# Performance work log

Hardware: AMD Instinct MI355X
Metric: run time of the kernel (lower is better)

The kernel has to match this reference:

```python
import jax, jax.numpy as jnp
import numpy as np

N = 50000
E = 800000
IN_DIM = 128
OUT_DIM = 128
EDGE_DIM = 3
H = 4
HD = OUT_DIM // H  # 32
SCALE = HD ** -0.5


def setup_inputs() -> dict:
    key = jax.random.key(0)
    ks = jax.random.split(key, 10)
    x = jax.random.normal(ks[0], (N, IN_DIM), dtype=jnp.float32)
    edge_index = jax.random.randint(ks[1], (2, E), 0, N, dtype=jnp.int64)
    edge_attr = jax.random.normal(ks[2], (E, EDGE_DIM), dtype=jnp.float32)
    s = 1.0 / np.sqrt(IN_DIM)
    Wq = jax.random.normal(ks[3], (IN_DIM, H * HD), dtype=jnp.float32) * s
    Wk = jax.random.normal(ks[4], (IN_DIM, H * HD), dtype=jnp.float32) * s
    Wv = jax.random.normal(ks[5], (IN_DIM, H * HD), dtype=jnp.float32) * s
    We = jax.random.normal(ks[6], (EDGE_DIM, H), dtype=jnp.float32) * (1.0 / np.sqrt(EDGE_DIM))
    Wo = jax.random.normal(ks[7], (H * HD, OUT_DIM), dtype=jnp.float32) * (1.0 / np.sqrt(H * HD))
    bo = jnp.zeros((OUT_DIM,), dtype=jnp.float32)
    Wm = jax.random.normal(ks[8], (IN_DIM + OUT_DIM, OUT_DIM), dtype=jnp.float32) * (1.0 / np.sqrt(IN_DIM + OUT_DIM))
    bm = jnp.zeros((OUT_DIM,), dtype=jnp.float32)
    return {"x": x, "edge_index": edge_index, "edge_attr": edge_attr,
            "Wq": Wq, "Wk": Wk, "Wv": Wv, "We": We, "Wo": Wo, "bo": bo,
            "Wm": Wm, "bm": bm}


def reference(x, edge_index, edge_attr, Wq, Wk, Wv, We, Wo, bo, Wm, bm):
    n = x.shape[0]
    src = edge_index[0]
    dst = edge_index[1]
    Q = (x @ Wq).reshape(n, H, HD)
    K = (x @ Wk).reshape(n, H, HD)
    V = (x @ Wv).reshape(n, H, HD)
    edge_bias = edge_attr @ We                                  # [E, H]
    attn = jnp.sum(Q[dst] * K[src], axis=-1) * SCALE + edge_bias  # [E, H]
    attn = jnp.where(attn >= 0, attn, 0.2 * attn)               # leaky_relu(0.2)
    # NOTE: original uses a single GLOBAL max over all edges/heads for stability
    attn_exp = jnp.exp(attn - jnp.max(attn))
    attn_sum = jax.ops.segment_sum(attn_exp, dst, num_segments=n)  # [N, H]
    attn_norm = attn_exp / jnp.maximum(attn_sum[dst], 1e-12)
    # dropout disabled (eval mode)
    weighted_V = V[src] * attn_norm[:, :, None]                 # [E, H, HD]
    agg = jax.ops.segment_sum(weighted_V, dst, num_segments=n)  # [N, H, HD]
    agg = agg.reshape(n, H * HD) @ Wo + bo                      # [N, OUT]
    h = jnp.concatenate([x, agg], axis=1) @ Wm + bm
    return jax.nn.relu(h)
```

## Files before the change

kernel.cpp:

```cpp
#include <hip/hip_runtime.h>
#include <hip/hip_bf16.h>
#include <math.h>

#define NN 50000
#define NE 800000
#define DIM 128
#define NH 4
#define HD 32
#define EH (NE * NH)
#define ATTN_SCALE 0.17677669529663687f
#define MTILE 64
#define GEMM_BLOCKS 782
#define NBKT 98
#define PTS 2048
#define PBLKS 391
#define HBLKS 104

typedef unsigned int uint;
typedef unsigned short ushort;
typedef __attribute__((ext_vector_type(8))) short short8;
typedef __attribute__((ext_vector_type(4))) float f32x4;

__device__ inline ushort f2bf(float f) {
    __hip_bfloat16 h = __float2bfloat16(f);
    return *(ushort*)&h;
}
__device__ inline float bflo(uint u) { return __uint_as_float(u << 16); }
__device__ inline float bfhi(uint u) { return __uint_as_float(u & 0xffff0000u); }

__global__ __launch_bounds__(256) void prep_x_kernel(
    const float* __restrict__ x, ushort* __restrict__ xb)
{
    const int i = blockIdx.x * 256 + threadIdx.x;
    const float4 v = ((const float4*)x)[i];
    ushort4 o;
    o.x = f2bf(v.x); o.y = f2bf(v.y); o.z = f2bf(v.z); o.w = f2bf(v.w);
    ((ushort4*)xb)[i] = o;
}

__global__ __launch_bounds__(128) void prep_wx_kernel(
    const float* __restrict__ Wo, const float* __restrict__ Wm,
    float* __restrict__ Wx)
{
    const int r = blockIdx.x, j = threadIdx.x;
    float acc = 0.f;
    for (int t = 0; t < 128; ++t)
        acc = fmaf(Wo[r * 128 + t], Wm[(128 + t) * 128 + j], acc);
    Wx[r * 128 + j] = acc;
}

__global__ __launch_bounds__(128) void prep_bias_kernel(
    const float* __restrict__ bo, const float* __restrict__ bm,
    const float* __restrict__ Wm, float* __restrict__ bprime)
{
    const int j = threadIdx.x;
    float acc = bm[j];
    for (int t = 0; t < 128; ++t)
        acc = fmaf(bo[t], Wm[(128 + t) * 128 + j], acc);
    bprime[j] = acc;
}

__global__ __launch_bounds__(256) void pack_qkv_kernel(
    const float* __restrict__ Wq, const float* __restrict__ Wk,
    const float* __restrict__ Wv, short* __restrict__ Bp)
{
    const int idx = blockIdx.x * 256 + threadIdx.x;
    const int j = idx & 7, lane = (idx >> 3) & 63;
    const int rest = idx >> 9;
    const int nt = rest % 24, kc = rest / 24;
    const int k = kc * 32 + (lane >> 4) * 8 + j;
    const int n = nt * 16 + (lane & 15);
    const float* W = (n < 128) ? Wq : (n < 256 ? Wk : Wv);
    Bp[idx] = (short)f2bf(W[k * 128 + (n & 127)]);
}

__global__ __launch_bounds__(256) void pack_out_kernel(
    const float* __restrict__ Wm, const float* __restrict__ Wx,
    short* __restrict__ Bp)
{
    const int idx = blockIdx.x * 256 + threadIdx.x;
    const int j = idx & 7, lane = (idx >> 3) & 63;
    const int rest = idx >> 9;
    const int nt = rest & 7, kc = rest >> 3;
    const int k = kc * 32 + (lane >> 4) * 8 + j;
    const int n = nt * 16 + (lane & 15);
    const float v = (k < 128) ? Wm[k * 128 + n] : Wx[(k - 128) * 128 + n];
    Bp[idx] = (short)f2bf(v);
}

__global__ __launch_bounds__(128) void bkt_zero_kernel(int* __restrict__ bkt_cnt)
{
    if (threadIdx.x < 128) bkt_cnt[threadIdx.x] = 0;
}

__global__ __launch_bounds__(256) void bkt_hist_kernel(
    const int* __restrict__ dst, int* __restrict__ bkt_cnt)
{
    __shared__ int c[NBKT];
    const int tid = threadIdx.x;
    if (tid < NBKT) c[tid] = 0;
    __syncthreads();
    for (int e = blockIdx.x * 256 + tid; e < NE; e += HBLKS * 256)
        atomicAdd(&c[dst[e] >> 9], 1);
    __syncthreads();
    if (tid < NBKT && c[tid]) atomicAdd(&bkt_cnt[tid], c[tid]);
}

__global__ void bkt_scan_kernel(const int* __restrict__ bkt_cnt,
                                int* __restrict__ bkt_base,
                                int* __restrict__ bkt_cursor,
                                int* __restrict__ rowptr)
{
    if (threadIdx.x == 0) {
        int run = 0;
        for (int b = 0; b < NBKT; ++b) {
            bkt_base[b] = run;
            bkt_cursor[b] = run;
            run += bkt_cnt[b];
        }
        bkt_base[NBKT] = run;
        rowptr[NN] = run;
    }
}

__global__ __launch_bounds__(256) void partition_kernel(
    const int* __restrict__ src, const int* __restrict__ dst,
    const float* __restrict__ edge_attr, const float* __restrict__ We,
    int* __restrict__ bkt_cursor,
    int* __restrict__ psrc, int* __restrict__ pdst, float* __restrict__ peb)
{
    __shared__ int cnt[NBKT], rbase[NBKT], cnt2[NBKT];
    const int tid = threadIdx.x;
    if (tid < NBKT) cnt[tid] = 0;
    __syncthreads();
    const int e0 = blockIdx.x * PTS;
    #pragma unroll
    for (int it = 0; it < 8; ++it) {
        const int e = e0 + it * 256 + tid;
        if (e < NE) atomicAdd(&cnt[dst[e] >> 9], 1);
    }
    __syncthreads();
    if (tid < NBKT) {
        rbase[tid] = cnt[tid] ? atomicAdd(&bkt_cursor[tid], cnt[tid]) : 0;
        cnt2[tid] = 0;
    }
    __syncthreads();
    #pragma unroll
    for (int it = 0; it < 8; ++it) {
        const int e = e0 + it * 256 + tid;
        if (e < NE) {
            const int d = dst[e];
            const int b = d >> 9;
            const int r = atomicAdd(&cnt2[b], 1);
            const int pos = rbase[b] + r;
            psrc[pos] = src[e];
            pdst[pos] = d;
            const float a0 = edge_attr[e * 3 + 0];
            const float a1 = edge_attr[e * 3 + 1];
            const float a2 = edge_attr[e * 3 + 2];
            float4 eb;
            eb.x = a0 * We[0] + a1 * We[4] + a2 * We[8];
            eb.y = a0 * We[1] + a1 * We[5] + a2 * We[9];
            eb.z = a0 * We[2] + a1 * We[6] + a2 * We[10];
            eb.w = a0 * We[3] + a1 * We[7] + a2 * We[11];
            *(float4*)(peb + (size_t)pos * 4) = eb;
        }
    }
}

__global__ __launch_bounds__(256) void bucket_csr_kernel(
    const int* __restrict__ bkt_base,
    const int* __restrict__ psrc, const int* __restrict__ pdst,
    const float* __restrict__ peb,
    int* __restrict__ rowptr,
    int* __restrict__ srcp, float* __restrict__ eb_csr)
{
    __shared__ int cnt[512];
    __shared__ int pre[512];
    __shared__ int sc[256];
    const int tid = threadIdx.x;
    const int b = blockIdx.x;
    const int base = bkt_base[b];
    const int n = bkt_base[b + 1] - base;
    const int node0 = b << 9;

    cnt[tid] = 0; cnt[tid + 256] = 0;
    __syncthreads();
    for (int i = base + tid; i < base + n; i += 256)
        atomicAdd(&cnt[pdst[i] - node0], 1);
    __syncthreads();

    const int pair = cnt[2 * tid] + cnt[2 * tid + 1];
    sc[tid] = pair;
    __syncthreads();
    for (int off = 1; off < 256; off <<= 1) {
        const int v = (tid >= off) ? sc[tid - off] : 0;
        __syncthreads();
        sc[tid] += v;
        __syncthreads();
    }
    const int ex = sc[tid] - pair;
    pre[2 * tid] = base + ex;
    pre[2 * tid + 1] = base + ex + cnt[2 * tid];
    __syncthreads();

    for (int l = tid; l < 512; l += 256) {
        const int g = node0 + l;
        if (g < NN) rowptr[g] = pre[l];
    }
    __syncthreads();

    for (int i = base + tid; i < base + n; i += 256) {
        const int d = pdst[i];
        const int pos = atomicAdd(&pre[d - node0], 1);
        srcp[pos] = psrc[i];
        *(float4*)(eb_csr + (size_t)pos * 4) =
            *(const float4*)(peb + (size_t)i * 4);
    }
}

__global__ __launch_bounds__(256) void qkv_mfma_kernel(
    const ushort* __restrict__ xb, const short* __restrict__ Bp,
    ushort* __restrict__ Qb, ushort* __restrict__ Kb, ushort* __restrict__ Vb)
{
    const int wave = threadIdx.x >> 6;
    const int lane = threadIdx.x & 63;
    const int m = lane & 15, quad = lane >> 4;
    const int row0w = blockIdx.x * MTILE + wave * 16;
    const int arow = row0w + m;
    const bool rowok = arow < NN;

    short8 a[4];
    #pragma unroll
    for (int kc = 0; kc < 4; ++kc)
        a[kc] = rowok ? *(const short8*)(xb + (size_t)arow * 128 + kc * 32 + quad * 8)
                      : (short8)(0);

    const int NT = 24;
    for (int nt = 0; nt < NT; nt += 2) {
        f32x4 acc0 = {0.f, 0.f, 0.f, 0.f}, acc1 = {0.f, 0.f, 0.f, 0.f};
        #pragma unroll
        for (int kc = 0; kc < 4; ++kc) {
            const short8 b0 = *(const short8*)(Bp + ((size_t)(kc * NT + nt) * 64 + lane) * 8);
            const short8 b1 = *(const short8*)(Bp + ((size_t)(kc * NT + nt + 1) * 64 + lane) * 8);
            acc0 = __builtin_amdgcn_mfma_f32_16x16x32_bf16(a[kc], b0, acc0, 0, 0, 0);
            acc1 = __builtin_amdgcn_mfma_f32_16x16x32_bf16(a[kc], b1, acc1, 0, 0, 0);
        }
        #pragma unroll
        for (int t = 0; t < 2; ++t) {
            const f32x4 acc = t ? acc1 : acc0;
            const int c = (nt + t) * 16 + m;
            ushort* dstp_ = (c < 128) ? Qb : (c < 256 ? Kb : Vb);
            const int lc = c & 127;
            #pragma unroll
            for (int g = 0; g < 4; ++g) {
                const int r = row0w + quad * 4 + g;
                if (r < NN) dstp_[(size_t)r * 128 + lc] = f2bf(acc[g]);
            }
        }
    }
}

__global__ __launch_bounds__(256) void out_mfma_kernel(
    const ushort* __restrict__ xb, const ushort* __restrict__ aggb,
    const short* __restrict__ Bp, const float* __restrict__ bprime,
    float* __restrict__ out)
{
    const int wave = threadIdx.x >> 6;
    const int lane = threadIdx.x & 63;
    const int m = lane & 15, quad = lane >> 4;
    const int row0w = blockIdx.x * MTILE + wave * 16;
    const int arow = row0w + m;
    const bool rowok = arow < NN;

    short8 a[8];
    #pragma unroll
    for (int kc = 0; kc < 4; ++kc)
        a[kc] = rowok ? *(const short8*)(xb + (size_t)arow * 128 + kc * 32 + quad * 8)
                      : (short8)(0);
    #pragma unroll
    for (int kc = 0; kc < 4; ++kc)
        a[4 + kc] = rowok ? *(const short8*)(aggb + (size_t)arow * 128 + kc * 32 + quad * 8)
                          : (short8)(0);

    const int NT = 8;
    for (int nt = 0; nt < NT; nt += 2) {
        f32x4 acc0 = {0.f, 0.f, 0.f, 0.f}, acc1 = {0.f, 0.f, 0.f, 0.f};
        #pragma unroll
        for (int kc = 0; kc < 8; ++kc) {
            const short8 b0 = *(const short8*)(Bp + ((size_t)(kc * NT + nt) * 64 + lane) * 8);
            const short8 b1 = *(const short8*)(Bp + ((size_t)(kc * NT + nt + 1) * 64 + lane) * 8);
            acc0 = __builtin_amdgcn_mfma_f32_16x16x32_bf16(a[kc], b0, acc0, 0, 0, 0);
            acc1 = __builtin_amdgcn_mfma_f32_16x16x32_bf16(a[kc], b1, acc1, 0, 0, 0);
        }
        #pragma unroll
        for (int t = 0; t < 2; ++t) {
            const f32x4 acc = t ? acc1 : acc0;
            const int c = (nt + t) * 16 + m;
            const float bb = bprime[c];
            #pragma unroll
            for (int g = 0; g < 4; ++g) {
                const int r = row0w + quad * 4 + g;
                if (r < NN) out[(size_t)r * 128 + c] = fmaxf(acc[g] + bb, 0.f);
            }
        }
    }
}

__global__ __launch_bounds__(256) void attn_agg_kernel(
    const ushort* __restrict__ Qb, const ushort* __restrict__ Kb,
    const ushort* __restrict__ Vb,
    const int* __restrict__ rowptr, const int* __restrict__ srcp,
    const float* __restrict__ eb_csr, ushort* __restrict__ aggb)
{
    const int tid = threadIdx.x;
    const int d = blockIdx.x * 4 + (tid >> 6);
    const int jj = tid & 63;
    const int h = jj >> 4;
    const int begin = rowptr[d];
    const int end   = rowptr[d + 1];

    const uint uq = *(const uint*)(Qb + (size_t)d * DIM + 2 * jj);
    const float q0 = bflo(uq), q1 = bfhi(uq);

    float ss0 = 0.f, ss1 = 0.f, ss2 = 0.f, ss3 = 0.f;
    float x0 = 0.f, x1 = 0.f, x2 = 0.f, x3 = 0.f;
    float y0 = 0.f, y1 = 0.f, y2 = 0.f, y3 = 0.f;

    int p = begin;
    for (; p + 4 <= end; p += 4) {
        const int s0 = srcp[p + 0];
        const int s1 = srcp[p + 1];
        const int s2 = srcp[p + 2];
        const int s3 = srcp[p + 3];
        const uint k0 = *(const uint*)(Kb + (size_t)s0 * DIM + 2 * jj);
        const uint k1 = *(const uint*)(Kb + (size_t)s1 * DIM + 2 * jj);
        const uint k2 = *(const uint*)(Kb + (size_t)s2 * DIM + 2 * jj);
        const uint k3 = *(const uint*)(Kb + (size_t)s3 * DIM + 2 * jj);
        float p0 = fmaf(q0, bflo(k0), q1 * bfhi(k0));
        float p1 = fmaf(q0, bflo(k1), q1 * bfhi(k1));
        float p2 = fmaf(q0, bflo(k2), q1 * bfhi(k2));
        float p3 = fmaf(q0, bflo(k3), q1 * bfhi(k3));
        #pragma unroll
        for (int m2 = 1; m2 <= 8; m2 <<= 1) {
            p0 += __shfl_xor(p0, m2);
            p1 += __shfl_xor(p1, m2);
            p2 += __shfl_xor(p2, m2);
            p3 += __shfl_xor(p3, m2);
        }
        float a0 = fmaf(p0, ATTN_SCALE, eb_csr[(size_t)(p + 0) * 4 + h]);
        float a1 = fmaf(p1, ATTN_SCALE, eb_csr[(size_t)(p + 1) * 4 + h]);
        float a2 = fmaf(p2, ATTN_SCALE, eb_csr[(size_t)(p + 2) * 4 + h]);
        float a3 = fmaf(p3, ATTN_SCALE, eb_csr[(size_t)(p + 3) * 4 + h]);
        a0 = (a0 >= 0.f) ? a0 : 0.2f * a0;
        a1 = (a1 >= 0.f) ? a1 : 0.2f * a1;
        a2 = (a2 >= 0.f) ? a2 : 0.2f * a2;
        a3 = (a3 >= 0.f) ? a3 : 0.2f * a3;
        const float w0 = __expf(a0);
        const float w1 = __expf(a1);
        const float w2 = __expf(a2);
        const float w3 = __expf(a3);
        const uint v0 = *(const uint*)(Vb + (size_t)s0 * DIM + 2 * jj);
        const uint v1 = *(const uint*)(Vb + (size_t)s1 * DIM + 2 * jj);
        const uint v2 = *(const uint*)(Vb + (size_t)s2 * DIM + 2 * jj);
        const uint v3 = *(const uint*)(Vb + (size_t)s3 * DIM + 2 * jj);
        ss0 += w0; ss1 += w1; ss2 += w2; ss3 += w3;
        x0 = fmaf(w0, bflo(v0), x0); y0 = fmaf(w0, bfhi(v0), y0);
        x1 = fmaf(w1, bflo(v1), x1); y1 = fmaf(w1, bfhi(v1), y1);
        x2 = fmaf(w2, bflo(v2), x2); y2 = fmaf(w2, bfhi(v2), y2);
        x3 = fmaf(w3, bflo(v3), x3); y3 = fmaf(w3, bfhi(v3), y3);
    }
    for (; p < end; ++p) {
        const int s = srcp[p];
        const uint uk = *(const uint*)(Kb + (size_t)s * DIM + 2 * jj);
        float part = fmaf(q0, bflo(uk), q1 * bfhi(uk));
        part += __shfl_xor(part, 1);
        part += __shfl_xor(part, 2);
        part += __shfl_xor(part, 4);
        part += __shfl_xor(part, 8);
        float a = fmaf(part, ATTN_SCALE, eb_csr[(size_t)p * 4 + h]);
        a = (a >= 0.f) ? a : 0.2f * a;
        const float w = __expf(a);
        const uint uv = *(const uint*)(Vb + (size_t)s * DIM + 2 * jj);
        ss0 += w;
        x0 = fmaf(w, bflo(uv), x0);
        y0 = fmaf(w, bfhi(uv), y0);
    }
    const float ssum = (ss0 + ss1) + (ss2 + ss3);
    const float inv = 1.f / fmaxf(ssum, 1e-12f);
    const float ax = ((x0 + x1) + (x2 + x3)) * inv;
    const float ay = ((y0 + y1) + (y2 + y3)) * inv;
    const uint packed = (uint)f2bf(ax) | ((uint)f2bf(ay) << 16);
    *(uint*)(aggb + (size_t)d * DIM + 2 * jj) = packed;
}

extern "C" void kernel_launch(void* const* d_in, const int* in_sizes, int n_in,
                              void* d_out, int out_size, void* d_ws, size_t ws_size,
                              hipStream_t stream)
{
    const float* x         = (const float*)d_in[0];
    const int*   edge_idx  = (const int*)d_in[1];
    const float* edge_attr = (const float*)d_in[2];
    const float* Wq        = (const float*)d_in[3];
    const float* Wk        = (const float*)d_in[4];
    const float* Wv        = (const float*)d_in[5];
    const float* We        = (const float*)d_in[6];
    const float* Wo        = (const float*)d_in[7];
    const float* bo        = (const float*)d_in[8];
    const float* Wm        = (const float*)d_in[9];
    const float* bm        = (const float*)d_in[10];
    float* out = (float*)d_out;

    const int* src = edge_idx;
    const int* dst = edge_idx + NE;

    ushort* xb   = (ushort*)d_ws;
    ushort* Qb   = xb + (size_t)NN * DIM;
    ushort* Kb   = Qb + (size_t)NN * DIM;
    ushort* Vb   = Kb + (size_t)NN * DIM;
    ushort* aggb = Vb + (size_t)NN * DIM;
    int*   psrc     = (int*)(aggb + (size_t)NN * DIM);
    int*   pdst     = psrc + NE;
    float* peb      = (float*)(pdst + NE);
    float* eb_csr   = peb + (size_t)EH;
    float* Wx       = eb_csr + (size_t)EH;
    float* bprime   = Wx + 16384;
    short* BpQKV    = (short*)(bprime + 128);
    short* BpOut    = BpQKV + 49152;
    int*   rowptr   = (int*)(BpOut + 32768);
    int*   srcp     = rowptr + 50048;
    int*   bkt_cnt    = srcp + NE;
    int*   bkt_base   = bkt_cnt + 128;
    int*   bkt_cursor = bkt_base + 128;

    prep_x_kernel<<<(NN * DIM / 4) / 256, 256, 0, stream>>>(x, xb);
    prep_wx_kernel<<<128, 128, 0, stream>>>(Wo, Wm, Wx);
    prep_bias_kernel<<<1, 128, 0, stream>>>(bo, bm, Wm, bprime);
    pack_qkv_kernel<<<192, 256, 0, stream>>>(Wq, Wk, Wv, BpQKV);
    pack_out_kernel<<<128, 256, 0, stream>>>(Wm, Wx, BpOut);

    bkt_zero_kernel<<<1, 128, 0, stream>>>(bkt_cnt);
    bkt_hist_kernel<<<HBLKS, 256, 0, stream>>>(dst, bkt_cnt);
    bkt_scan_kernel<<<1, 64, 0, stream>>>(bkt_cnt, bkt_base, bkt_cursor, rowptr);
    partition_kernel<<<PBLKS, 256, 0, stream>>>(src, dst, edge_attr, We,
                                                bkt_cursor, psrc, pdst, peb);
    bucket_csr_kernel<<<NBKT, 256, 0, stream>>>(bkt_base, psrc, pdst, peb,
                                                rowptr, srcp, eb_csr);

    qkv_mfma_kernel<<<GEMM_BLOCKS, 256, 0, stream>>>(xb, BpQKV, Qb, Kb, Vb);
    attn_agg_kernel<<<NN / 4, 256, 0, stream>>>(Qb, Kb, Vb, rowptr, srcp,
                                                eb_csr, aggb);
    out_mfma_kernel<<<GEMM_BLOCKS, 256, 0, stream>>>(xb, aggb, BpOut, bprime, out);
}
```

Baseline: 294.3 us.

## Split wavefront into four edge groups with 16-byte K/V loads per lane

The attention-aggregation kernel now has each 64-lane wavefront handle four edges at once, one per 16-lane group, with each lane loading 8 bf16 values (uint4) of K and V instead of 2. The per-head dot product needs only two shuffle steps, and the groups' partial sums are combined with cross-group shuffles at the end. The next edge's source index and edge bias are prefetched one iteration ahead, and the scalar tail loop is replaced by masking. This cuts per-edge load instruction count and shuffle work and exposes more memory parallelism, at the cost of more registers and a final reduction.

```diff
diff --git a/kernel.cpp b/kernel.cpp
--- a/kernel.cpp
+++ b/kernel.cpp
@@ -315,83 +315,93 @@
 {
     const int tid = threadIdx.x;
     const int d = blockIdx.x * 4 + (tid >> 6);
-    const int jj = tid & 63;
-    const int h = jj >> 4;
+    const int lane = tid & 63;
+    const int g = lane >> 4;
+    const int t = lane & 15;
+    const int h = t >> 2;
     const int begin = rowptr[d];
     const int end   = rowptr[d + 1];
 
-    const uint uq = *(const uint*)(Qb + (size_t)d * DIM + 2 * jj);
-    const float q0 = bflo(uq), q1 = bfhi(uq);
-
-    float ss0 = 0.f, ss1 = 0.f, ss2 = 0.f, ss3 = 0.f;
-    float x0 = 0.f, x1 = 0.f, x2 = 0.f, x3 = 0.f;
-    float y0 = 0.f, y1 = 0.f, y2 = 0.f, y3 = 0.f;
-
-    int p = begin;
-    for (; p + 4 <= end; p += 4) {
-        const int s0 = srcp[p + 0];
-        const int s1 = srcp[p + 1];
-        const int s2 = srcp[p + 2];
-        const int s3 = srcp[p + 3];
-        const uint k0 = *(const uint*)(Kb + (size_t)s0 * DIM + 2 * jj);
-        const uint k1 = *(const uint*)(Kb + (size_t)s1 * DIM + 2 * jj);
-        const uint k2 = *(const uint*)(Kb + (size_t)s2 * DIM + 2 * jj);
-        const uint k3 = *(const uint*)(Kb + (size_t)s3 * DIM + 2 * jj);
-        float p0 = fmaf(q0, bflo(k0), q1 * bfhi(k0));
-        float p1 = fmaf(q0, bflo(k1), q1 * bfhi(k1));
-        float p2 = fmaf(q0, bflo(k2), q1 * bfhi(k2));
-        float p3 = fmaf(q0, bflo(k3), q1 * bfhi(k3));
-        #pragma unroll
-        for (int m2 = 1; m2 <= 8; m2 <<= 1) {
-            p0 += __shfl_xor(p0, m2);
-            p1 += __shfl_xor(p1, m2);
-            p2 += __shfl_xor(p2, m2);
-            p3 += __shfl_xor(p3, m2);
-        }
-        float a0 = fmaf(p0, ATTN_SCALE, eb_csr[(size_t)(p + 0) * 4 + h]);
-        float a1 = fmaf(p1, ATTN_SCALE, eb_csr[(size_t)(p + 1) * 4 + h]);
-        float a2 = fmaf(p2, ATTN_SCALE, eb_csr[(size_t)(p + 2) * 4 + h]);
-        float a3 = fmaf(p3, ATTN_SCALE, eb_csr[(size_t)(p + 3) * 4 + h]);
-        a0 = (a0 >= 0.f) ? a0 : 0.2f * a0;
-        a1 = (a1 >= 0.f) ? a1 : 0.2f * a1;
-        a2 = (a2 >= 0.f) ? a2 : 0.2f * a2;
-        a3 = (a3 >= 0.f) ? a3 : 0.2f * a3;
-        const float w0 = __expf(a0);
-        const float w1 = __expf(a1);
-        const float w2 = __expf(a2);
-        const float w3 = __expf(a3);
-        const uint v0 = *(const uint*)(Vb + (size_t)s0 * DIM + 2 * jj);
-        const uint v1 = *(const uint*)(Vb + (size_t)s1 * DIM + 2 * jj);
-        const uint v2 = *(const uint*)(Vb + (size_t)s2 * DIM + 2 * jj);
-        const uint v3 = *(const uint*)(Vb + (size_t)s3 * DIM + 2 * jj);
-        ss0 += w0; ss1 += w1; ss2 += w2; ss3 += w3;
-        x0 = fmaf(w0, bflo(v0), x0); y0 = fmaf(w0, bfhi(v0), y0);
-        x1 = fmaf(w1, bflo(v1), x1); y1 = fmaf(w1, bfhi(v1), y1);
-        x2 = fmaf(w2, bflo(v2), x2); y2 = fmaf(w2, bfhi(v2), y2);
-        x3 = fmaf(w3, bflo(v3), x3); y3 = fmaf(w3, bfhi(v3), y3);
-    }
-    for (; p < end; ++p) {
-        const int s = srcp[p];
-        const uint uk = *(const uint*)(Kb + (size_t)s * DIM + 2 * jj);
-        float part = fmaf(q0, bflo(uk), q1 * bfhi(uk));
-        part += __shfl_xor(part, 1);
-        part += __shfl_xor(part, 2);
-        part += __shfl_xor(part, 4);
-        part += __shfl_xor(part, 8);
-        float a = fmaf(part, ATTN_SCALE, eb_csr[(size_t)p * 4 + h]);
-        a = (a >= 0.f) ? a : 0.2f * a;
-        const float w = __expf(a);
-        const uint uv = *(const uint*)(Vb + (size_t)s * DIM + 2 * jj);
-        ss0 += w;
-        x0 = fmaf(w, bflo(uv), x0);
-        y0 = fmaf(w, bfhi(uv), y0);
-    }
-    const float ssum = (ss0 + ss1) + (ss2 + ss3);
-    const float inv = 1.f / fmaxf(ssum, 1e-12f);
-    const float ax = ((x0 + x1) + (x2 + x3)) * inv;
-    const float ay = ((y0 + y1) + (y2 + y3)) * inv;
-    const uint packed = (uint)f2bf(ax) | ((uint)f2bf(ay) << 16);
-    *(uint*)(aggb + (size_t)d * DIM + 2 * jj) = packed;
+    const uint4 uq = *(const uint4*)(Qb + (size_t)d * DIM + 8 * t);
+    float q0 = bflo(uq.x), q1 = bfhi(uq.x);
+    float q2 = bflo(uq.y), q3 = bfhi(uq.y);
+    float q4 = bflo(uq.z), q5 = bfhi(uq.z);
+    float q6 = bflo(uq.w), q7 = bfhi(uq.w);
+
+    float ss = 0.f;
+    float a0 = 0.f, a1 = 0.f, a2 = 0.f, a3 = 0.f;
+    float a4 = 0.f, a5 = 0.f, a6 = 0.f, a7 = 0.f;
+
+    if (begin < end) {
+        int ec = begin + g;
+        if (ec >= end) ec = end - 1;
+        int s   = srcp[ec];
+        float eb = eb_csr[(size_t)ec * 4 + h];
+
+        for (int p = begin; p < end; p += 4) {
+            const bool ok = (p + g) < end;
+            const int pn = p + 4;
+            int sn = s; float ebn = eb;
+            if (pn < end) {
+                int en = pn + g;
+                if (en >= end) en = end - 1;
+                sn  = srcp[en];
+                ebn = eb_csr[(size_t)en * 4 + h];
+            }
+
+            const uint4 uk = *(const uint4*)(Kb + (size_t)s * DIM + 8 * t);
+            const uint4 uv = *(const uint4*)(Vb + (size_t)s * DIM + 8 * t);
+
+            float da = q0 * bflo(uk.x);
+            float db = q1 * bfhi(uk.x);
+            da = fmaf(q2, bflo(uk.y), da);
+            db = fmaf(q3, bfhi(uk.y), db);
+            da = fmaf(q4, bflo(uk.z), da);
+            db = fmaf(q5, bfhi(uk.z), db);
+            da = fmaf(q6, bflo(uk.w), da);
+            db = fmaf(q7, bfhi(uk.w), db);
+            float part = da + db;
+            part += __shfl_xor(part, 1);
+            part += __shfl_xor(part, 2);
+
+            float a = fmaf(part, ATTN_SCALE, eb);
+            a = (a >= 0.f) ? a : 0.2f * a;
+            float w = ok ? __expf(a) : 0.f;
+
+            ss += w;
+            a0 = fmaf(w, bflo(uv.x), a0);
+            a1 = fmaf(w, bfhi(uv.x), a1);
+            a2 = fmaf(w, bflo(uv.y), a2);
+            a3 = fmaf(w, bfhi(uv.y), a3);
+            a4 = fmaf(w, bflo(uv.z), a4);
+            a5 = fmaf(w, bfhi(uv.z), a5);
+            a6 = fmaf(w, bflo(uv.w), a6);
+            a7 = fmaf(w, bfhi(uv.w), a7);
+
+            s = sn; eb = ebn;
+        }
+    }
+
+    ss += __shfl_xor(ss, 16);
+    ss += __shfl_xor(ss, 32);
+    a0 += __shfl_xor(a0, 16); a0 += __shfl_xor(a0, 32);
+    a1 += __shfl_xor(a1, 16); a1 += __shfl_xor(a1, 32);
+    a2 += __shfl_xor(a2, 16); a2 += __shfl_xor(a2, 32);
+    a3 += __shfl_xor(a3, 16); a3 += __shfl_xor(a3, 32);
+    a4 += __shfl_xor(a4, 16); a4 += __shfl_xor(a4, 32);
+    a5 += __shfl_xor(a5, 16); a5 += __shfl_xor(a5, 32);
+    a6 += __shfl_xor(a6, 16); a6 += __shfl_xor(a6, 32);
+    a7 += __shfl_xor(a7, 16); a7 += __shfl_xor(a7, 32);
+
+    if (g == 0) {
+        const float inv = 1.f / fmaxf(ss, 1e-12f);
+        uint4 o;
+        o.x = (uint)f2bf(a0 * inv) | ((uint)f2bf(a1 * inv) << 16);
+        o.y = (uint)f2bf(a2 * inv) | ((uint)f2bf(a3 * inv) << 16);
+        o.z = (uint)f2bf(a4 * inv) | ((uint)f2bf(a5 * inv) << 16);
+        o.w = (uint)f2bf(a6 * inv) | ((uint)f2bf(a7 * inv) << 16);
+        *(uint4*)(aggb + (size_t)d * DIM + 8 * t) = o;
+    }
 }
 
 extern "C" void kernel_launch(void* const* d_in, const int* in_sizes, int n_in,
```

New measurement: 287.5 us. 2.3% less time.
